# Optimization experiments

Measured on AMD Instinct MI355X. Metric: run time of the kernel, lower is better.

Reference implementation:

```python
import jax, jax.numpy as jnp
import numpy as np

B, T, D = 2, 2048, 1024
H, M = 8, 64
KD = D // H   # head_k_dim = head_v_dim = 128
EPS = 1e-5
GATE_NORM = 16.0


def setup_inputs() -> dict:
    key = jax.random.key(0)
    ks = jax.random.split(key, 7)
    sc = 0.02  # ~ xavier_uniform with gain 2**-2.5
    return {
        "hidden_states": jax.random.normal(ks[0], (B, T, D), jnp.float32),
        "Wq": jax.random.normal(ks[1], (D, D), jnp.float32) * sc,
        "Wk": jax.random.normal(ks[2], (D, D), jnp.float32) * sc,
        "Wv": jax.random.normal(ks[3], (D, D), jnp.float32) * sc,
        "Wf": jax.random.normal(ks[4], (H * M, D), jnp.float32) * sc,
        "Wo": jax.random.normal(ks[5], (D, D), jnp.float32) * sc,
        "g_weight": jnp.ones((D,), jnp.float32),
    }


def swish(x):
    return x * jax.nn.sigmoid(x)


def gated_abc_scan(q, k, v, s, g):
    """Gated ABC slot-memory recurrence.
    q,k: [B,H,T,K]; v: [B,H,T,V]; s,g: [B,H,T,M] (g is log forget gate).
    hk_t = hk_{t-1}*exp(g_t) + k_t (x) s_t            [B,H,K,M]
    p_t  = softmax(scale * q_t . hk_t, over slots M)
    hv_t = hv_{t-1}*exp(g_t) + s_t (x) v_t            [B,H,M,V]
    o_t  = p_t . hv_t
    """
    scale = q.shape[-1] ** -0.5
    qT = jnp.moveaxis(q, 2, 0) * scale  # [T,B,H,K]
    kT = jnp.moveaxis(k, 2, 0)
    vT = jnp.moveaxis(v, 2, 0)
    sT = jnp.moveaxis(s, 2, 0)
    gT = jnp.moveaxis(g, 2, 0)
    Bb, Hh, _, K = q.shape
    V, Mm = v.shape[-1], s.shape[-1]
    hk0 = jnp.zeros((Bb, Hh, K, Mm), q.dtype)
    hv0 = jnp.zeros((Bb, Hh, Mm, V), q.dtype)

    def step(carry, xs):
        hk, hv = carry
        qi, ki, vi, si, gi = xs
        ge = jnp.exp(gi)  # [B,H,M]
        hk = hk * ge[..., None, :] + ki[..., None] * si[..., None, :]
        p = jax.nn.softmax(jnp.einsum('bhk,bhkm->bhm', qi, hk), axis=-1)
        hv = hv * ge[..., None] + si[..., None] * vi[..., None, :]
        oi = jnp.einsum('bhm,bhmv->bhv', p, hv)
        return (hk, hv), oi

    _, oT = jax.lax.scan(step, (hk0, hv0), (qT, kT, vT, sT, gT))
    return jnp.moveaxis(oT, 0, 2)  # [B,H,T,V]


def reference(hidden_states, Wq, Wk, Wv, Wf, Wo, g_weight):
    x = hidden_states
    q = x @ Wq.T   # [B,T,D]
    k = x @ Wk.T
    v = x @ Wv.T
    f = x @ Wf.T   # [B,T,H*M]

    # b t (h d) -> b h t d
    q = jnp.moveaxis(q.reshape(B, T, H, KD), 2, 1)
    k = jnp.moveaxis(k.reshape(B, T, H, KD), 2, 1)
    v = jnp.moveaxis(v.reshape(B, T, H, KD), 2, 1)
    f = jnp.moveaxis(f.reshape(B, T, H, M), 2, 1)

    # feature map: swish on q, k, v
    q, k, v = swish(q), swish(k), swish(v)

    # log forget gate and input gate
    g = jax.nn.log_sigmoid(f) / GATE_NORM   # [B,H,T,M], <= 0
    s = 1.0 - jnp.exp(g)

    o = gated_abc_scan(q, k, v, s, g)       # [B,H,T,KD]
    o = jnp.moveaxis(o, 1, 2).reshape(B, T, D)  # b h t d -> b t (h d)

    # use_norm and not use_output_gate: swish -> RMSNorm(weight) -> o_proj
    o = swish(o)
    rms = o * jax.lax.rsqrt(jnp.mean(o * o, axis=-1, keepdims=True) + EPS)
    o = (rms * g_weight) @ Wo.T
    return o
```

## Files before the change

kernel.cpp:

```cpp
#include <hip/hip_runtime.h>
#include <cstddef>
#include <cstdint>

namespace {

constexpr int Bc = 2, Tc = 2048, Dc = 1024, Hc = 8, Mc = 64, KDc = 128;
constexpr int ROWS = Bc * Tc;
constexpr int CH = 64, NC = Tc / CH;
constexpr float SCALE = 0.08838834764831845f;
constexpr float GATE_NORM_INV = 1.0f / 16.0f;

typedef __attribute__((ext_vector_type(8))) short bf16x8;
typedef __attribute__((ext_vector_type(4))) float f32x4;

__device__ __forceinline__ float swishf(float x) {
  return x / (1.0f + __expf(-x));
}
__device__ __forceinline__ float logsig16f(float x) {
  return (fminf(x, 0.f) - __logf(1.f + __expf(-fabsf(x)))) * GATE_NORM_INV;
}
__device__ __forceinline__ unsigned short f2bf(float f) {
  union { float f; unsigned u; } v; v.f = f;
  unsigned r = v.u + 0x7FFF + ((v.u >> 16) & 1);
  return (unsigned short)(r >> 16);
}
__device__ __forceinline__ void fma4(float a, const float4& b, float4& acc) {
  acc.x = fmaf(a, b.x, acc.x); acc.y = fmaf(a, b.y, acc.y);
  acc.z = fmaf(a, b.z, acc.z); acc.w = fmaf(a, b.w, acc.w);
}
__device__ __forceinline__ float dot4acc(const float4& a, const float4& b, float c) {
  c = fmaf(a.x, b.x, c); c = fmaf(a.y, b.y, c);
  c = fmaf(a.z, b.z, c); c = fmaf(a.w, b.w, c);
  return c;
}

#define GLOAD_LDS16(g, l) __builtin_amdgcn_global_load_lds( \
    (const __attribute__((address_space(1))) unsigned int*)(g), \
    (__attribute__((address_space(3))) unsigned int*)(l), 16, 0, 0)

__global__ __launch_bounds__(256)
void cvt_bf16_all(const float* __restrict__ x, const float* __restrict__ wq,
                  const float* __restrict__ wk, const float* __restrict__ wv,
                  const float* __restrict__ wf, const float* __restrict__ wo,
                  unsigned short* __restrict__ xb, unsigned short* __restrict__ wqkvf,
                  unsigned short* __restrict__ wob)
{
  long e = ((long)blockIdx.x * 256 + threadIdx.x) * 8;
  const float* src; unsigned short* dst; long off;
  if (e < 4194304L)      { src = x;  dst = xb;              off = e; }
  else if (e < 5242880L) { src = wq; dst = wqkvf;           off = e - 4194304L; }
  else if (e < 6291456L) { src = wk; dst = wqkvf + 1048576; off = e - 5242880L; }
  else if (e < 7340032L) { src = wv; dst = wqkvf + 2097152; off = e - 6291456L; }
  else if (e < 7864320L) { src = wf; dst = wqkvf + 3145728; off = e - 7340032L; }
  else                   { src = wo; dst = wob;             off = e - 7864320L; }
  float4 a = *(const float4*)(src + off);
  float4 b = *(const float4*)(src + off + 4);
  ushort4 h0, h1;
  h0.x = f2bf(a.x); h0.y = f2bf(a.y); h0.z = f2bf(a.z); h0.w = f2bf(a.w);
  h1.x = f2bf(b.x); h1.y = f2bf(b.y); h1.z = f2bf(b.z); h1.w = f2bf(b.w);
  *(ushort4*)(dst + off) = h0;
  *(ushort4*)(dst + off + 4) = h1;
}

template<int EPI>
__global__ __launch_bounds__(256)
void gemm_bt(const unsigned short* __restrict__ A, const unsigned short* __restrict__ Bm,
             float* __restrict__ C0, float* __restrict__ C1,
             float* __restrict__ C2, float* __restrict__ C3)
{
  __shared__ __align__(16) unsigned short As[128 * 32];
  __shared__ __align__(16) unsigned short Bs[128 * 32];
  const int tid = threadIdx.x;
  const int lane = tid & 63, w = tid >> 6;
  const int bcol = (int)blockIdx.x, brow = (int)blockIdx.y;
  const int wr = w >> 1, wc = w & 1;
  const int lrow = lane & 15, lk8 = (lane >> 4) << 3;

  const int srow = w * 32 + (lane >> 2);
  const int scol = (lane & 3) << 3;
  const unsigned short* Ag0 = A + (size_t)(brow * 128 + srow) * 1024 + scol;
  const unsigned short* Ag1 = Ag0 + (size_t)16 * 1024;
  const unsigned short* Bg0 = Bm + (size_t)(bcol * 128 + srow) * 1024 + scol;
  const unsigned short* Bg1 = Bg0 + (size_t)16 * 1024;
  unsigned short* Al0 = As + w * 1024;
  unsigned short* Al1 = As + w * 1024 + 512;
  unsigned short* Bl0 = Bs + w * 1024;
  unsigned short* Bl1 = Bs + w * 1024 + 512;

  f32x4 acc[4][4];
#pragma unroll
  for (int i = 0; i < 4; ++i)
#pragma unroll
    for (int j = 0; j < 4; ++j)
#pragma unroll
      for (int r = 0; r < 4; ++r) acc[i][j][r] = 0.f;

  for (int k0 = 0; k0 < 1024; k0 += 32) {
    __syncthreads();
    GLOAD_LDS16(Ag0 + k0, Al0);
    GLOAD_LDS16(Ag1 + k0, Al1);
    GLOAD_LDS16(Bg0 + k0, Bl0);
    GLOAD_LDS16(Bg1 + k0, Bl1);
    __syncthreads();

    bf16x8 av[4], bv[4];
#pragma unroll
    for (int i = 0; i < 4; ++i)
      av[i] = *(const bf16x8*)&As[(wr * 64 + i * 16 + lrow) * 32 + lk8];
#pragma unroll
    for (int j = 0; j < 4; ++j)
      bv[j] = *(const bf16x8*)&Bs[(wc * 64 + j * 16 + lrow) * 32 + lk8];
#pragma unroll
    for (int i = 0; i < 4; ++i)
#pragma unroll
      for (int j = 0; j < 4; ++j)
        acc[i][j] = __builtin_amdgcn_mfma_f32_16x16x32_bf16(av[i], bv[j], acc[i][j], 0, 0, 0);
  }

#pragma unroll
  for (int i = 0; i < 4; ++i) {
#pragma unroll
    for (int j = 0; j < 4; ++j) {
#pragma unroll
      for (int r = 0; r < 4; ++r) {
        int row = brow * 128 + wr * 64 + i * 16 + ((lane >> 4) << 2) + r;
        int n   = bcol * 128 + wc * 64 + j * 16 + (lane & 15);
        float v = acc[i][j][r];
        if (EPI == 0) {
          C0[(size_t)row * 1024 + n] = v;
        } else {
          if (n < 1024)      C0[(size_t)row * 1024 + n]          = swishf(v);
          else if (n < 2048) C1[(size_t)row * 1024 + (n - 1024)] = swishf(v);
          else if (n < 3072) C2[(size_t)row * 1024 + (n - 2048)] = swishf(v);
          else               C3[(size_t)row * 512  + (n - 3072)] = logsig16f(v);
        }
      }
    }
  }
}

__global__ __launch_bounds__(256)
void scan_phase1(const float* __restrict__ K_, const float* __restrict__ V_,
                 const float* __restrict__ G_, float* __restrict__ St,
                 float* __restrict__ Gc)
{
  __shared__ __align__(16) float uls[CH][68];
  __shared__ __align__(16) float Bb[CH][132];
  __shared__ float egcs[CH];
  const int tid = threadIdx.x;
  const int c = (int)blockIdx.x, bh = (int)blockIdx.y;
  const int b = bh >> 3, h = bh & 7;
  const int t0 = c * CH;

  {
    const int gr = tid >> 2, gc0 = (tid & 3) << 4;
    const float* gsrc = G_ + (size_t)(b * Tc + t0 + gr) * (Hc * Mc) + h * Mc + gc0;
#pragma unroll
    for (int j = 0; j < 4; ++j)
      *(float4*)&uls[gr][gc0 + 4 * j] = *(const float4*)(gsrc + 4 * j);
  }
  {
    const float* ksrc = K_ + (size_t)(b * Tc + t0) * Dc + h * KDc;
#pragma unroll
    for (int j = 0; j < 8; ++j) {
      int fi = tid + j * 256;
      int r = fi >> 5, cc = (fi & 31) << 2;
      *(float4*)&Bb[r][cc] = *(const float4*)(ksrc + (size_t)r * Dc + cc);
    }
  }
  __syncthreads();
  if (tid < CH) {
    float run = 0.f;
    for (int t = 0; t < CH; ++t) {
      float gv = uls[t][tid];
      run += gv;
      uls[t][tid] = (1.0f - __expf(gv)) * __expf(-run);
    }
    float eg = __expf(run);
    egcs[tid] = eg;
    Gc[((size_t)bh * NC + c) * CH + tid] = eg;
  }
  __syncthreads();
  const size_t stbase = ((size_t)bh * NC + c) * 16384;
  {
    const int k0 = (tid >> 3) << 2, m0 = (tid & 7) << 3;
    float4 acc[4][2];
#pragma unroll
    for (int i = 0; i < 4; ++i) { acc[i][0] = make_float4(0,0,0,0); acc[i][1] = make_float4(0,0,0,0); }
    for (int tau = 0; tau < CH; ++tau) {
      float4 kv = *(const float4*)&Bb[tau][k0];
      float4 u0 = *(const float4*)&uls[tau][m0];
      float4 u1 = *(const float4*)&uls[tau][m0 + 4];
      fma4(kv.x, u0, acc[0][0]); fma4(kv.x, u1, acc[0][1]);
      fma4(kv.y, u0, acc[1][0]); fma4(kv.y, u1, acc[1][1]);
      fma4(kv.z, u0, acc[2][0]); fma4(kv.z, u1, acc[2][1]);
      fma4(kv.w, u0, acc[3][0]); fma4(kv.w, u1, acc[3][1]);
    }
    float4 e0 = *(const float4*)&egcs[m0];
    float4 e1 = *(const float4*)&egcs[m0 + 4];
#pragma unroll
    for (int i = 0; i < 4; ++i) {
      float4 o0, o1;
      o0.x = acc[i][0].x * e0.x; o0.y = acc[i][0].y * e0.y; o0.z = acc[i][0].z * e0.z; o0.w = acc[i][0].w * e0.w;
      o1.x = acc[i][1].x * e1.x; o1.y = acc[i][1].y * e1.y; o1.z = acc[i][1].z * e1.z; o1.w = acc[i][1].w * e1.w;
      float* dst = St + stbase + (size_t)(k0 + i) * 64 + m0;
      *(float4*)dst = o0; *(float4*)(dst + 4) = o1;
    }
  }
  __syncthreads();
  {
    const float* vsrc = V_ + (size_t)(b * Tc + t0) * Dc + h * KDc;
#pragma unroll
    for (int j = 0; j < 8; ++j) {
      int fi = tid + j * 256;
      int r = fi >> 5, cc = (fi & 31) << 2;
      *(float4*)&Bb[r][cc] = *(const float4*)(vsrc + (size_t)r * Dc + cc);
    }
  }
  __syncthreads();
  {
    const int m0 = (tid >> 4) << 2, v0 = (tid & 15) << 3;
    float4 acc[4][2];
#pragma unroll
    for (int i = 0; i < 4; ++i) { acc[i][0] = make_float4(0,0,0,0); acc[i][1] = make_float4(0,0,0,0); }
    for (int tau = 0; tau < CH; ++tau) {
      float4 u4 = *(const float4*)&uls[tau][m0];
      float4 va = *(const float4*)&Bb[tau][v0];
      float4 vb = *(const float4*)&Bb[tau][v0 + 4];
      fma4(u4.x, va, acc[0][0]); fma4(u4.x, vb, acc[0][1]);
      fma4(u4.y, va, acc[1][0]); fma4(u4.y, vb, acc[1][1]);
      fma4(u4.z, va, acc[2][0]); fma4(u4.z, vb, acc[2][1]);
      fma4(u4.w, va, acc[3][0]); fma4(u4.w, vb, acc[3][1]);
    }
#pragma unroll
    for (int i = 0; i < 4; ++i) {
      float eg = egcs[m0 + i];
      float4 o0 = acc[i][0], o1 = acc[i][1];
      o0.x *= eg; o0.y *= eg; o0.z *= eg; o0.w *= eg;
      o1.x *= eg; o1.y *= eg; o1.z *= eg; o1.w *= eg;
      float* dst = St + stbase + 8192 + (size_t)(m0 + i) * 128 + v0;
      *(float4*)dst = o0; *(float4*)(dst + 4) = o1;
    }
  }
}

__global__ __launch_bounds__(256)
void scan_phase2(float* St, const float* __restrict__ Gc)
{
  const int tid = threadIdx.x;
  const int bh = (int)blockIdx.x, slice = (int)blockIdx.y;
  const int e0 = slice * 1024 + tid * 4;
  const bool isHk = e0 < 8192;
  float* base = St + (size_t)bh * NC * 16384 + e0;
  const float* gcp = Gc + (size_t)bh * NC * CH;
  float4 run = make_float4(0, 0, 0, 0);
  float4 d = *(float4*)base;
  for (int c = 0; c < NC; ++c) {
    float4 dn = make_float4(0, 0, 0, 0);
    if (c + 1 < NC) dn = *(float4*)(base + (size_t)(c + 1) * 16384);
    float4 ge;
    if (isHk) {
      ge = *(const float4*)(gcp + c * CH + (e0 & 63));
    } else {
      float g1 = gcp[c * CH + ((e0 - 8192) >> 7)];
      ge = make_float4(g1, g1, g1, g1);
    }
    *(float4*)(base + (size_t)c * 16384) = run;
    run.x = fmaf(run.x, ge.x, d.x);
    run.y = fmaf(run.y, ge.y, d.y);
    run.z = fmaf(run.z, ge.z, d.z);
    run.w = fmaf(run.w, ge.w, d.w);
    d = dn;
  }
}

__global__ __launch_bounds__(256)
void scan_phase3(const float* __restrict__ Q_, const float* __restrict__ K_,
                 const float* __restrict__ V_, const float* __restrict__ G_,
                 const float* __restrict__ St, float* __restrict__ O_)
{
  __shared__ __align__(16) float Qs[CH][132];
  __shared__ __align__(16) float Bf[8704];
  __shared__ __align__(16) float us[CH][68];
  __shared__ __align__(16) float es[CH][68];
  __shared__ __align__(16) float Ss[CH][68];
  __shared__ __align__(16) float Ps[CH][68];

  const int tid = threadIdx.x;
  const int c = (int)blockIdx.x, bh = (int)blockIdx.y;
  const int b = bh >> 3, h = bh & 7;
  const int t0 = c * CH;
  const size_t stbase = ((size_t)bh * NC + c) * 16384;

  {
    const int gr = tid >> 2, gc0 = (tid & 3) << 4;
    const float* gsrc = G_ + (size_t)(b * Tc + t0 + gr) * (Hc * Mc) + h * Mc + gc0;
#pragma unroll
    for (int j = 0; j < 4; ++j)
      *(float4*)&es[gr][gc0 + 4 * j] = *(const float4*)(gsrc + 4 * j);
    const float* qsrc = Q_ + (size_t)(b * Tc + t0) * Dc + h * KDc;
    const float* ksrc = K_ + (size_t)(b * Tc + t0) * Dc + h * KDc;
#pragma unroll
    for (int j = 0; j < 8; ++j) {
      int fi = tid + j * 256;
      int r = fi >> 5, cc4 = (fi & 31) << 2;
      *(float4*)&Qs[r][cc4] = *(const float4*)(qsrc + (size_t)r * Dc + cc4);
      *(float4*)&Bf[r * 132 + cc4] = *(const float4*)(ksrc + (size_t)r * Dc + cc4);
    }
  }
  __syncthreads();
  if (tid < CH) {
    float run = 0.f;
    for (int t = 0; t < CH; ++t) {
      float gv = es[t][tid];
      run += gv;
      us[t][tid] = (1.0f - __expf(gv)) * __expf(-run);
      es[t][tid] = __expf(run);
    }
  }
  const int tt = tid >> 4, ccg = tid & 15;
  {
    const int tr = tt << 2, tc = ccg << 2;
    float4 acc[4];
#pragma unroll
    for (int i = 0; i < 4; ++i) acc[i] = make_float4(0, 0, 0, 0);
    for (int k = 0; k < KDc; k += 4) {
      float4 kr0 = *(const float4*)&Bf[(tc + 0) * 132 + k];
      float4 kr1 = *(const float4*)&Bf[(tc + 1) * 132 + k];
      float4 kr2 = *(const float4*)&Bf[(tc + 2) * 132 + k];
      float4 kr3 = *(const float4*)&Bf[(tc + 3) * 132 + k];
#pragma unroll
      for (int i = 0; i < 4; ++i) {
        float4 qi = *(const float4*)&Qs[tr + i][k];
        acc[i].x = dot4acc(qi, kr0, acc[i].x);
        acc[i].y = dot4acc(qi, kr1, acc[i].y);
        acc[i].z = dot4acc(qi, kr2, acc[i].z);
        acc[i].w = dot4acc(qi, kr3, acc[i].w);
      }
    }
#pragma unroll
    for (int i = 0; i < 4; ++i) {
      float4 w;
      w.x = (tc + 0 <= tr + i) ? acc[i].x : 0.f;
      w.y = (tc + 1 <= tr + i) ? acc[i].y : 0.f;
      w.z = (tc + 2 <= tr + i) ? acc[i].z : 0.f;
      w.w = (tc + 3 <= tr + i) ? acc[i].w : 0.f;
      *(float4*)&Ss[tr + i][tc] = w;
    }
  }
  __syncthreads();
  {
#pragma unroll
    for (int j = 0; j < 8; ++j) {
      int fi = tid + j * 256;
      int k = fi >> 4, m4 = (fi & 15) << 2;
      *(float4*)&Bf[k * 68 + m4] = *(const float4*)(St + stbase + (size_t)k * 64 + m4);
    }
  }
  __syncthreads();
  {
    const int tr = tt << 2, m0 = ccg << 2;
    float4 acc[4];
#pragma unroll
    for (int i = 0; i < 4; ++i) acc[i] = make_float4(0, 0, 0, 0);
    for (int tau = 0; tau < CH; tau += 4) {
      float4 u0 = *(const float4*)&us[tau + 0][m0];
      float4 u1 = *(const float4*)&us[tau + 1][m0];
      float4 u2 = *(const float4*)&us[tau + 2][m0];
      float4 u3 = *(const float4*)&us[tau + 3][m0];
#pragma unroll
      for (int i = 0; i < 4; ++i) {
        float4 s4 = *(const float4*)&Ss[tr + i][tau];
        fma4(s4.x, u0, acc[i]); fma4(s4.y, u1, acc[i]);
        fma4(s4.z, u2, acc[i]); fma4(s4.w, u3, acc[i]);
      }
    }
    for (int k = 0; k < KDc; k += 4) {
      float4 h0 = *(const float4*)&Bf[(k + 0) * 68 + m0];
      float4 h1 = *(const float4*)&Bf[(k + 1) * 68 + m0];
      float4 h2 = *(const float4*)&Bf[(k + 2) * 68 + m0];
      float4 h3 = *(const float4*)&Bf[(k + 3) * 68 + m0];
#pragma unroll
      for (int i = 0; i < 4; ++i) {
        float4 q4 = *(const float4*)&Qs[tr + i][k];
        fma4(q4.x, h0, acc[i]); fma4(q4.y, h1, acc[i]);
        fma4(q4.z, h2, acc[i]); fma4(q4.w, h3, acc[i]);
      }
    }
#pragma unroll
    for (int i = 0; i < 4; ++i) {
      float4 ev = *(const float4*)&es[tr + i][m0];
      float4 ov;
      ov.x = SCALE * ev.x * acc[i].x;
      ov.y = SCALE * ev.y * acc[i].y;
      ov.z = SCALE * ev.z * acc[i].z;
      ov.w = SCALE * ev.w * acc[i].w;
      *(float4*)&Ps[tr + i][m0] = ov;
    }
  }
  __syncthreads();
  {
    const int row = tid >> 2, m0 = (tid & 3) << 4;
    float4 a0 = *(const float4*)&Ps[row][m0];
    float4 a1 = *(const float4*)&Ps[row][m0 + 4];
    float4 a2 = *(const float4*)&Ps[row][m0 + 8];
    float4 a3 = *(const float4*)&Ps[row][m0 + 12];
    float mx = fmaxf(fmaxf(fmaxf(a0.x, a0.y), fmaxf(a0.z, a0.w)),
                     fmaxf(fmaxf(a1.x, a1.y), fmaxf(a1.z, a1.w)));
    mx = fmaxf(mx, fmaxf(fmaxf(fmaxf(a2.x, a2.y), fmaxf(a2.z, a2.w)),
                         fmaxf(fmaxf(a3.x, a3.y), fmaxf(a3.z, a3.w))));
    mx = fmaxf(mx, __shfl_xor(mx, 1, 64));
    mx = fmaxf(mx, __shfl_xor(mx, 2, 64));
    a0.x = __expf(a0.x - mx); a0.y = __expf(a0.y - mx); a0.z = __expf(a0.z - mx); a0.w = __expf(a0.w - mx);
    a1.x = __expf(a1.x - mx); a1.y = __expf(a1.y - mx); a1.z = __expf(a1.z - mx); a1.w = __expf(a1.w - mx);
    a2.x = __expf(a2.x - mx); a2.y = __expf(a2.y - mx); a2.z = __expf(a2.z - mx); a2.w = __expf(a2.w - mx);
    a3.x = __expf(a3.x - mx); a3.y = __expf(a3.y - mx); a3.z = __expf(a3.z - mx); a3.w = __expf(a3.w - mx);
    float sm = a0.x + a0.y + a0.z + a0.w + a1.x + a1.y + a1.z + a1.w
             + a2.x + a2.y + a2.z + a2.w + a3.x + a3.y + a3.z + a3.w;
    sm += __shfl_xor(sm, 1, 64);
    sm += __shfl_xor(sm, 2, 64);
    float inv = 1.0f / sm;
    float4 e0 = *(const float4*)&es[row][m0];
    float4 e1 = *(const float4*)&es[row][m0 + 4];
    float4 e2 = *(const float4*)&es[row][m0 + 8];
    float4 e3 = *(const float4*)&es[row][m0 + 12];
    a0.x *= inv * e0.x; a0.y *= inv * e0.y; a0.z *= inv * e0.z; a0.w *= inv * e0.w;
    a1.x *= inv * e1.x; a1.y *= inv * e1.y; a1.z *= inv * e1.z; a1.w *= inv * e1.w;
    a2.x *= inv * e2.x; a2.y *= inv * e2.y; a2.z *= inv * e2.z; a2.w *= inv * e2.w;
    a3.x *= inv * e3.x; a3.y *= inv * e3.y; a3.z *= inv * e3.z; a3.w *= inv * e3.w;
    *(float4*)&Ss[row][m0] = a0;
    *(float4*)&Ss[row][m0 + 4] = a1;
    *(float4*)&Ss[row][m0 + 8] = a2;
    *(float4*)&Ss[row][m0 + 12] = a3;
  }
  {
    const float* vsrc = V_ + (size_t)(b * Tc + t0) * Dc + h * KDc;
#pragma unroll
    for (int j = 0; j < 8; ++j) {
      int fi = tid + j * 256;
      int r = fi >> 5, cc4 = (fi & 31) << 2;
      *(float4*)&Bf[r * 132 + cc4] = *(const float4*)(vsrc + (size_t)r * Dc + cc4);
    }
  }
  __syncthreads();
  {
    const int tr = tt << 2, tc = ccg << 2;
    float4 acc[4];
#pragma unroll
    for (int i = 0; i < 4; ++i) acc[i] = make_float4(0, 0, 0, 0);
    for (int m = 0; m < CH; m += 4) {
      float4 u0 = *(const float4*)&us[tc + 0][m];
      float4 u1 = *(const float4*)&us[tc + 1][m];
      float4 u2 = *(const float4*)&us[tc + 2][m];
      float4 u3 = *(const float4*)&us[tc + 3][m];
#pragma unroll
      for (int i = 0; i < 4; ++i) {
        float4 w4 = *(const float4*)&Ss[tr + i][m];
        acc[i].x = dot4acc(w4, u0, acc[i].x);
        acc[i].y = dot4acc(w4, u1, acc[i].y);
        acc[i].z = dot4acc(w4, u2, acc[i].z);
        acc[i].w = dot4acc(w4, u3, acc[i].w);
      }
    }
#pragma unroll
    for (int i = 0; i < 4; ++i) {
      float4 w;
      w.x = (tc + 0 <= tr + i) ? acc[i].x : 0.f;
      w.y = (tc + 1 <= tr + i) ? acc[i].y : 0.f;
      w.z = (tc + 2 <= tr + i) ? acc[i].z : 0.f;
      w.w = (tc + 3 <= tr + i) ? acc[i].w : 0.f;
      *(float4*)&Ps[tr + i][tc] = w;
    }
  }
  __syncthreads();
  const int tr = tt << 2, v0 = ccg << 3;
  float4 accO[4][2];
#pragma unroll
  for (int i = 0; i < 4; ++i) { accO[i][0] = make_float4(0,0,0,0); accO[i][1] = make_float4(0,0,0,0); }
  for (int tau = 0; tau < CH; tau += 4) {
    float4 pr[4];
#pragma unroll
    for (int i = 0; i < 4; ++i) pr[i] = *(const float4*)&Ps[tr + i][tau];
#pragma unroll
    for (int d = 0; d < 4; ++d) {
      float4 va = *(const float4*)&Bf[(tau + d) * 132 + v0];
      float4 vb = *(const float4*)&Bf[(tau + d) * 132 + v0 + 4];
#pragma unroll
      for (int i = 0; i < 4; ++i) {
        float p = (d == 0) ? pr[i].x : (d == 1) ? pr[i].y : (d == 2) ? pr[i].z : pr[i].w;
        fma4(p, va, accO[i][0]); fma4(p, vb, accO[i][1]);
      }
    }
  }
  __syncthreads();
  {
#pragma unroll
    for (int j = 0; j < 8; ++j) {
      int fi = tid + j * 256;
      int m = fi >> 5, c4 = (fi & 31) << 2;
      *(float4*)&Bf[m * 132 + c4] = *(const float4*)(St + stbase + 8192 + (size_t)m * 128 + c4);
    }
  }
  __syncthreads();
  for (int m = 0; m < CH; m += 4) {
    float4 wr[4];
#pragma unroll
    for (int i = 0; i < 4; ++i) wr[i] = *(const float4*)&Ss[tr + i][m];
#pragma unroll
    for (int d = 0; d < 4; ++d) {
      float4 ha = *(const float4*)&Bf[(m + d) * 132 + v0];
      float4 hb = *(const float4*)&Bf[(m + d) * 132 + v0 + 4];
#pragma unroll
      for (int i = 0; i < 4; ++i) {
        float w = (d == 0) ? wr[i].x : (d == 1) ? wr[i].y : (d == 2) ? wr[i].z : wr[i].w;
        fma4(w, ha, accO[i][0]); fma4(w, hb, accO[i][1]);
      }
    }
  }
#pragma unroll
  for (int i = 0; i < 4; ++i) {
    float* dst = O_ + (size_t)(b * Tc + t0 + tr + i) * Dc + h * KDc + v0;
    *(float4*)dst = accO[i][0];
    *(float4*)(dst + 4) = accO[i][1];
  }
}

__global__ __launch_bounds__(256)
void post_rms(const float* __restrict__ Oin, const float* __restrict__ gw,
              unsigned short* __restrict__ Nout)
{
  __shared__ float red[4];
  const int row = (int)blockIdx.x, tid = threadIdx.x;
  const float4 o4 = *(const float4*)(Oin + (size_t)row * Dc + tid * 4);
  float4 s4;
  s4.x = swishf(o4.x); s4.y = swishf(o4.y); s4.z = swishf(o4.z); s4.w = swishf(o4.w);
  float ss = s4.x * s4.x + s4.y * s4.y + s4.z * s4.z + s4.w * s4.w;
#pragma unroll
  for (int off = 32; off > 0; off >>= 1) ss += __shfl_xor(ss, off, 64);
  if ((tid & 63) == 0) red[tid >> 6] = ss;
  __syncthreads();
  float total = red[0] + red[1] + red[2] + red[3];
  float rms = rsqrtf(total * (1.0f / Dc) + 1e-5f);
  const float4 g4 = *(const float4*)(gw + tid * 4);
  ushort4 h;
  h.x = f2bf(s4.x * rms * g4.x);
  h.y = f2bf(s4.y * rms * g4.y);
  h.z = f2bf(s4.z * rms * g4.z);
  h.w = f2bf(s4.w * rms * g4.w);
  *(ushort4*)(Nout + (size_t)row * Dc + tid * 4) = h;
}

}

extern "C" void kernel_launch(void* const* d_in, const int* in_sizes, int n_in,
                              void* d_out, int out_size, void* d_ws, size_t ws_size,
                              hipStream_t stream)
{
  const float* x  = (const float*)d_in[0];
  const float* Wq = (const float*)d_in[1];
  const float* Wk = (const float*)d_in[2];
  const float* Wv = (const float*)d_in[3];
  const float* Wf = (const float*)d_in[4];
  const float* Wo = (const float*)d_in[5];
  const float* gw = (const float*)d_in[6];
  float* out = (float*)d_out;

  char* ws = (char*)d_ws;
  const size_t MB = 1ull << 20;
  float* qb  = (float*)(ws);
  float* kb  = (float*)(ws + 16 * MB);
  float* vb  = (float*)(ws + 32 * MB);
  float* gb  = (float*)(ws + 48 * MB);
  float* st  = (float*)(ws + 56 * MB);
  float* gcb = (float*)(ws + 88 * MB);
  float* ob  = (float*)(ws + 89 * MB);
  unsigned short* xb    = (unsigned short*)(ws + 56 * MB);
  unsigned short* wqkvf = (unsigned short*)(ws + 64 * MB);
  unsigned short* wob   = (unsigned short*)(ws + 105 * MB);
  unsigned short* nbb   = (unsigned short*)(ws);

  dim3 blk(256);
  cvt_bf16_all<<<dim3(4352), blk, 0, stream>>>(x, Wq, Wk, Wv, Wf, Wo, xb, wqkvf, wob);
  gemm_bt<1><<<dim3(28, 32), blk, 0, stream>>>(xb, wqkvf, qb, kb, vb, gb);
  scan_phase1<<<dim3(NC, 16), blk, 0, stream>>>(kb, vb, gb, st, gcb);
  scan_phase2<<<dim3(16, 16), blk, 0, stream>>>(st, gcb);
  scan_phase3<<<dim3(NC, 16), blk, 0, stream>>>(qb, kb, vb, gb, st, ob);
  post_rms<<<dim3(ROWS), blk, 0, stream>>>(ob, gw, nbb);
  gemm_bt<0><<<dim3(8, 32), blk, 0, stream>>>(nbb, wob, out, nullptr, nullptr, nullptr);
}
```

Baseline: 318.2 us.

## Move chunked scan intra-chunk matmuls to bf16 MFMA with transposed state layout

Rewrites scan_phase3 so its intra-chunk products (QK^T, S·u, Q·hk, W·u, P·V, W·hv) run as bf16 16x16x32 MFMA ops instead of scalar fp32 FMA loops. Inputs and chunk states are converted to bf16 in LDS. To give MFMA operands a contiguous K dimension, phase1 now stores chunk states transposed (hk as [M][K], hv as [V][M]), and phase2's gate indexing is changed to match. The goal is to cut the cost of the FP32 ALU work in the per-chunk kernel. In exchange it loses precision from bf16 rounding of activations, states and probabilities, and adds conversion overhead and scattered scalar output stores.

New measurement: 266.9 us. 1.19x faster.

```diff
diff --git a/kernel.cpp b/kernel.cpp
--- a/kernel.cpp
+++ b/kernel.cpp
@@ -28,10 +28,8 @@
   acc.x = fmaf(a, b.x, acc.x); acc.y = fmaf(a, b.y, acc.y);
   acc.z = fmaf(a, b.z, acc.z); acc.w = fmaf(a, b.w, acc.w);
 }
-__device__ __forceinline__ float dot4acc(const float4& a, const float4& b, float c) {
-  c = fmaf(a.x, b.x, c); c = fmaf(a.y, b.y, c);
-  c = fmaf(a.z, b.z, c); c = fmaf(a.w, b.w, c);
-  return c;
+__device__ __forceinline__ float getc(const float4& v, int c) {
+  return (c == 0) ? v.x : (c == 1) ? v.y : (c == 2) ? v.z : v.w;
 }
 
 #define GLOAD_LDS16(g, l) __builtin_amdgcn_global_load_lds( \
@@ -196,15 +194,16 @@
       fma4(kv.z, u0, acc[2][0]); fma4(kv.z, u1, acc[2][1]);
       fma4(kv.w, u0, acc[3][0]); fma4(kv.w, u1, acc[3][1]);
     }
-    float4 e0 = *(const float4*)&egcs[m0];
-    float4 e1 = *(const float4*)&egcs[m0 + 4];
-#pragma unroll
-    for (int i = 0; i < 4; ++i) {
-      float4 o0, o1;
-      o0.x = acc[i][0].x * e0.x; o0.y = acc[i][0].y * e0.y; o0.z = acc[i][0].z * e0.z; o0.w = acc[i][0].w * e0.w;
-      o1.x = acc[i][1].x * e1.x; o1.y = acc[i][1].y * e1.y; o1.z = acc[i][1].z * e1.z; o1.w = acc[i][1].w * e1.w;
-      float* dst = St + stbase + (size_t)(k0 + i) * 64 + m0;
-      *(float4*)dst = o0; *(float4*)(dst + 4) = o1;
+#pragma unroll
+    for (int jm = 0; jm < 8; ++jm) {
+      int m = m0 + jm, hh = jm >> 2, cc = jm & 3;
+      float eg = egcs[m];
+      float4 o;
+      o.x = getc(acc[0][hh], cc) * eg;
+      o.y = getc(acc[1][hh], cc) * eg;
+      o.z = getc(acc[2][hh], cc) * eg;
+      o.w = getc(acc[3][hh], cc) * eg;
+      *(float4*)(St + stbase + (size_t)m * 128 + k0) = o;
     }
   }
   __syncthreads();
@@ -232,14 +231,16 @@
       fma4(u4.z, va, acc[2][0]); fma4(u4.z, vb, acc[2][1]);
       fma4(u4.w, va, acc[3][0]); fma4(u4.w, vb, acc[3][1]);
     }
-#pragma unroll
-    for (int i = 0; i < 4; ++i) {
-      float eg = egcs[m0 + i];
-      float4 o0 = acc[i][0], o1 = acc[i][1];
-      o0.x *= eg; o0.y *= eg; o0.z *= eg; o0.w *= eg;
-      o1.x *= eg; o1.y *= eg; o1.z *= eg; o1.w *= eg;
-      float* dst = St + stbase + 8192 + (size_t)(m0 + i) * 128 + v0;
-      *(float4*)dst = o0; *(float4*)(dst + 4) = o1;
+    float4 e4 = *(const float4*)&egcs[m0];
+#pragma unroll
+    for (int jv = 0; jv < 8; ++jv) {
+      int v = v0 + jv, hh = jv >> 2, cc = jv & 3;
+      float4 o;
+      o.x = getc(acc[0][hh], cc) * e4.x;
+      o.y = getc(acc[1][hh], cc) * e4.y;
+      o.z = getc(acc[2][hh], cc) * e4.z;
+      o.w = getc(acc[3][hh], cc) * e4.w;
+      *(float4*)(St + stbase + 8192 + (size_t)v * 64 + m0) = o;
     }
   }
 }
@@ -260,10 +261,10 @@
     if (c + 1 < NC) dn = *(float4*)(base + (size_t)(c + 1) * 16384);
     float4 ge;
     if (isHk) {
-      ge = *(const float4*)(gcp + c * CH + (e0 & 63));
+      float g1 = gcp[c * CH + (e0 >> 7)];
+      ge = make_float4(g1, g1, g1, g1);
     } else {
-      float g1 = gcp[c * CH + ((e0 - 8192) >> 7)];
-      ge = make_float4(g1, g1, g1, g1);
+      ge = *(const float4*)(gcp + c * CH + ((e0 - 8192) & 63));
     }
     *(float4*)(base + (size_t)c * 16384) = run;
     run.x = fmaf(run.x, ge.x, d.x);
@@ -279,250 +280,228 @@
                  const float* __restrict__ V_, const float* __restrict__ G_,
                  const float* __restrict__ St, float* __restrict__ O_)
 {
-  __shared__ __align__(16) float Qs[CH][132];
-  __shared__ __align__(16) float Bf[8704];
-  __shared__ __align__(16) float us[CH][68];
-  __shared__ __align__(16) float es[CH][68];
-  __shared__ __align__(16) float Ss[CH][68];
-  __shared__ __align__(16) float Ps[CH][68];
-
-  const int tid = threadIdx.x;
+  __shared__ __align__(16) unsigned short Qb[64 * 136];
+  __shared__ __align__(16) unsigned short buf2[128 * 72];
+  __shared__ __align__(16) unsigned short Sb[64 * 72];
+  __shared__ __align__(16) unsigned short Wb[64 * 72];
+  __shared__ __align__(16) unsigned short P2b[64 * 72];
+  __shared__ __align__(16) unsigned short ub[64 * 72];
+  __shared__ __align__(16) unsigned short ubt[64 * 72];
+  __shared__ __align__(16) float es[64 * 68];
+
+  const int tid = threadIdx.x, lane = tid & 63, w = tid >> 6;
   const int c = (int)blockIdx.x, bh = (int)blockIdx.y;
   const int b = bh >> 3, h = bh & 7;
   const int t0 = c * CH;
   const size_t stbase = ((size_t)bh * NC + c) * 16384;
-
-  {
-    const int gr = tid >> 2, gc0 = (tid & 3) << 4;
-    const float* gsrc = G_ + (size_t)(b * Tc + t0 + gr) * (Hc * Mc) + h * Mc + gc0;
-#pragma unroll
-    for (int j = 0; j < 4; ++j)
-      *(float4*)&es[gr][gc0 + 4 * j] = *(const float4*)(gsrc + 4 * j);
-    const float* qsrc = Q_ + (size_t)(b * Tc + t0) * Dc + h * KDc;
-    const float* ksrc = K_ + (size_t)(b * Tc + t0) * Dc + h * KDc;
+  const int col = lane & 15, rb = (lane >> 4) << 2;
+  const int arow = lane & 15, ak = (lane >> 4) << 3;
+
+  {
+    const int r = tid >> 2, cs = (tid & 3) << 5;
+    const float* qs = Q_ + (size_t)(b * Tc + t0 + r) * Dc + h * KDc + cs;
+    const float* ks = K_ + (size_t)(b * Tc + t0 + r) * Dc + h * KDc + cs;
+#pragma unroll
+    for (int q = 0; q < 8; ++q) {
+      float4 a = *(const float4*)(qs + q * 4);
+      ushort4 ha; ha.x = f2bf(a.x); ha.y = f2bf(a.y); ha.z = f2bf(a.z); ha.w = f2bf(a.w);
+      *(ushort4*)&Qb[r * 136 + cs + q * 4] = ha;
+      float4 bq = *(const float4*)(ks + q * 4);
+      ushort4 hb; hb.x = f2bf(bq.x); hb.y = f2bf(bq.y); hb.z = f2bf(bq.z); hb.w = f2bf(bq.w);
+      *(ushort4*)&buf2[r * 136 + cs + q * 4] = hb;
+    }
+    const int gcs = (tid & 3) << 4;
+    const float* gs = G_ + (size_t)(b * Tc + t0 + r) * (Hc * Mc) + h * Mc + gcs;
+#pragma unroll
+    for (int q = 0; q < 4; ++q)
+      *(float4*)&es[r * 68 + gcs + q * 4] = *(const float4*)(gs + q * 4);
+  }
+  __syncthreads();
+  if (tid < 64) {
+    float run = 0.f;
+    ushort4 pk;
+    for (int t = 0; t < 64; ++t) {
+      float gv = es[t * 68 + tid];
+      run += gv;
+      float uu = (1.0f - __expf(gv)) * __expf(-run);
+      es[t * 68 + tid] = __expf(run);
+      unsigned short ubf = f2bf(uu);
+      ub[t * 72 + tid] = ubf;
+      ((unsigned short*)&pk)[t & 3] = ubf;
+      if ((t & 3) == 3) *(ushort4*)&ubt[tid * 72 + (t - 3)] = pk;
+    }
+  }
+  __syncthreads();
+  {
+    f32x4 s[4];
+#pragma unroll
+    for (int j = 0; j < 4; ++j)
+#pragma unroll
+      for (int r = 0; r < 4; ++r) s[j][r] = 0.f;
+#pragma unroll
+    for (int k0 = 0; k0 < 128; k0 += 32) {
+      bf16x8 aq = *(const bf16x8*)&Qb[(w * 16 + arow) * 136 + k0 + ak];
+#pragma unroll
+      for (int j = 0; j < 4; ++j) {
+        bf16x8 bk = *(const bf16x8*)&buf2[(j * 16 + arow) * 136 + k0 + ak];
+        s[j] = __builtin_amdgcn_mfma_f32_16x16x32_bf16(aq, bk, s[j], 0, 0, 0);
+      }
+    }
+#pragma unroll
+    for (int j = 0; j < 4; ++j)
+#pragma unroll
+      for (int r = 0; r < 4; ++r) {
+        int t = w * 16 + rb + r, tau = j * 16 + col;
+        Sb[t * 72 + tau] = f2bf((tau <= t) ? s[j][r] : 0.f);
+      }
+  }
+  __syncthreads();
+  {
+    const int r = tid >> 2, cs = (tid & 3) << 5;
+    const float* hs = St + stbase + (size_t)r * 128 + cs;
+#pragma unroll
+    for (int q = 0; q < 8; ++q) {
+      float4 a = *(const float4*)(hs + q * 4);
+      ushort4 ha; ha.x = f2bf(a.x); ha.y = f2bf(a.y); ha.z = f2bf(a.z); ha.w = f2bf(a.w);
+      *(ushort4*)&buf2[r * 136 + cs + q * 4] = ha;
+    }
+  }
+  __syncthreads();
+  {
+    f32x4 a4[4];
+#pragma unroll
+    for (int j = 0; j < 4; ++j)
+#pragma unroll
+      for (int r = 0; r < 4; ++r) a4[j][r] = 0.f;
+#pragma unroll
+    for (int k0 = 0; k0 < 64; k0 += 32) {
+      bf16x8 as_ = *(const bf16x8*)&Sb[(w * 16 + arow) * 72 + k0 + ak];
+#pragma unroll
+      for (int j = 0; j < 4; ++j) {
+        bf16x8 bu = *(const bf16x8*)&ubt[(j * 16 + arow) * 72 + k0 + ak];
+        a4[j] = __builtin_amdgcn_mfma_f32_16x16x32_bf16(as_, bu, a4[j], 0, 0, 0);
+      }
+    }
+#pragma unroll
+    for (int k0 = 0; k0 < 128; k0 += 32) {
+      bf16x8 aq = *(const bf16x8*)&Qb[(w * 16 + arow) * 136 + k0 + ak];
+#pragma unroll
+      for (int j = 0; j < 4; ++j) {
+        bf16x8 bh_ = *(const bf16x8*)&buf2[(j * 16 + arow) * 136 + k0 + ak];
+        a4[j] = __builtin_amdgcn_mfma_f32_16x16x32_bf16(aq, bh_, a4[j], 0, 0, 0);
+      }
+    }
+    float er[4][4], lg[4][4];
+#pragma unroll
+    for (int j = 0; j < 4; ++j)
+#pragma unroll
+      for (int r = 0; r < 4; ++r) {
+        er[j][r] = es[(w * 16 + rb + r) * 68 + j * 16 + col];
+        lg[j][r] = SCALE * er[j][r] * a4[j][r];
+      }
+    float mx[4] = {-1e30f, -1e30f, -1e30f, -1e30f};
+#pragma unroll
+    for (int j = 0; j < 4; ++j)
+#pragma unroll
+      for (int r = 0; r < 4; ++r) mx[r] = fmaxf(mx[r], lg[j][r]);
+#pragma unroll
+    for (int bx = 1; bx < 16; bx <<= 1)
+#pragma unroll
+      for (int r = 0; r < 4; ++r) mx[r] = fmaxf(mx[r], __shfl_xor(mx[r], bx, 64));
+    float se[4] = {0.f, 0.f, 0.f, 0.f}, p[4][4];
+#pragma unroll
+    for (int j = 0; j < 4; ++j)
+#pragma unroll
+      for (int r = 0; r < 4; ++r) { p[j][r] = __expf(lg[j][r] - mx[r]); se[r] += p[j][r]; }
+#pragma unroll
+    for (int bx = 1; bx < 16; bx <<= 1)
+#pragma unroll
+      for (int r = 0; r < 4; ++r) se[r] += __shfl_xor(se[r], bx, 64);
+#pragma unroll
+    for (int j = 0; j < 4; ++j)
+#pragma unroll
+      for (int r = 0; r < 4; ++r) {
+        float wv = p[j][r] / se[r] * er[j][r];
+        Wb[(w * 16 + rb + r) * 72 + j * 16 + col] = f2bf(wv);
+      }
+  }
+  __syncthreads();
+  {
+#pragma unroll
+    for (int q = 0; q < 8; ++q) {
+      int fi = tid + q * 256;
+      int tau = fi & 63, v0 = (fi >> 6) << 2;
+      float4 a = *(const float4*)(V_ + (size_t)(b * Tc + t0 + tau) * Dc + h * KDc + v0);
+      buf2[(v0 + 0) * 72 + tau] = f2bf(a.x);
+      buf2[(v0 + 1) * 72 + tau] = f2bf(a.y);
+      buf2[(v0 + 2) * 72 + tau] = f2bf(a.z);
+      buf2[(v0 + 3) * 72 + tau] = f2bf(a.w);
+    }
+  }
+  {
+    f32x4 p2[4];
+#pragma unroll
+    for (int j = 0; j < 4; ++j)
+#pragma unroll
+      for (int r = 0; r < 4; ++r) p2[j][r] = 0.f;
+#pragma unroll
+    for (int k0 = 0; k0 < 64; k0 += 32) {
+      bf16x8 aw = *(const bf16x8*)&Wb[(w * 16 + arow) * 72 + k0 + ak];
+#pragma unroll
+      for (int j = 0; j < 4; ++j) {
+        bf16x8 bu = *(const bf16x8*)&ub[(j * 16 + arow) * 72 + k0 + ak];
+        p2[j] = __builtin_amdgcn_mfma_f32_16x16x32_bf16(aw, bu, p2[j], 0, 0, 0);
+      }
+    }
+#pragma unroll
+    for (int j = 0; j < 4; ++j)
+#pragma unroll
+      for (int r = 0; r < 4; ++r) {
+        int t = w * 16 + rb + r, tau = j * 16 + col;
+        P2b[t * 72 + tau] = f2bf((tau <= t) ? p2[j][r] : 0.f);
+      }
+  }
+  __syncthreads();
+  f32x4 o8[8];
+#pragma unroll
+  for (int j = 0; j < 8; ++j)
+#pragma unroll
+    for (int r = 0; r < 4; ++r) o8[j][r] = 0.f;
+#pragma unroll
+  for (int k0 = 0; k0 < 64; k0 += 32) {
+    bf16x8 ap = *(const bf16x8*)&P2b[(w * 16 + arow) * 72 + k0 + ak];
 #pragma unroll
     for (int j = 0; j < 8; ++j) {
-      int fi = tid + j * 256;
-      int r = fi >> 5, cc4 = (fi & 31) << 2;
-      *(float4*)&Qs[r][cc4] = *(const float4*)(qsrc + (size_t)r * Dc + cc4);
-      *(float4*)&Bf[r * 132 + cc4] = *(const float4*)(ksrc + (size_t)r * Dc + cc4);
-    }
-  }
-  __syncthreads();
-  if (tid < CH) {
-    float run = 0.f;
-    for (int t = 0; t < CH; ++t) {
-      float gv = es[t][tid];
-      run += gv;
-      us[t][tid] = (1.0f - __expf(gv)) * __expf(-run);
-      es[t][tid] = __expf(run);
-    }
-  }
-  const int tt = tid >> 4, ccg = tid & 15;
-  {
-    const int tr = tt << 2, tc = ccg << 2;
-    float4 acc[4];
-#pragma unroll
-    for (int i = 0; i < 4; ++i) acc[i] = make_float4(0, 0, 0, 0);
-    for (int k = 0; k < KDc; k += 4) {
-      float4 kr0 = *(const float4*)&Bf[(tc + 0) * 132 + k];
-      float4 kr1 = *(const float4*)&Bf[(tc + 1) * 132 + k];
-      float4 kr2 = *(const float4*)&Bf[(tc + 2) * 132 + k];
-      float4 kr3 = *(const float4*)&Bf[(tc + 3) * 132 + k];
-#pragma unroll
-      for (int i = 0; i < 4; ++i) {
-        float4 qi = *(const float4*)&Qs[tr + i][k];
-        acc[i].x = dot4acc(qi, kr0, acc[i].x);
-        acc[i].y = dot4acc(qi, kr1, acc[i].y);
-        acc[i].z = dot4acc(qi, kr2, acc[i].z);
-        acc[i].w = dot4acc(qi, kr3, acc[i].w);
-      }
-    }
-#pragma unroll
-    for (int i = 0; i < 4; ++i) {
-      float4 w;
-      w.x = (tc + 0 <= tr + i) ? acc[i].x : 0.f;
-      w.y = (tc + 1 <= tr + i) ? acc[i].y : 0.f;
-      w.z = (tc + 2 <= tr + i) ? acc[i].z : 0.f;
-      w.w = (tc + 3 <= tr + i) ? acc[i].w : 0.f;
-      *(float4*)&Ss[tr + i][tc] = w;
-    }
-  }
-  __syncthreads();
-  {
+      bf16x8 bv = *(const bf16x8*)&buf2[(j * 16 + arow) * 72 + k0 + ak];
+      o8[j] = __builtin_amdgcn_mfma_f32_16x16x32_bf16(ap, bv, o8[j], 0, 0, 0);
+    }
+  }
+  __syncthreads();
+  {
+    const int r = tid >> 1, cs = (tid & 1) << 5;
+    const float* hs = St + stbase + 8192 + (size_t)r * 64 + cs;
+#pragma unroll
+    for (int q = 0; q < 8; ++q) {
+      float4 a = *(const float4*)(hs + q * 4);
+      ushort4 ha; ha.x = f2bf(a.x); ha.y = f2bf(a.y); ha.z = f2bf(a.z); ha.w = f2bf(a.w);
+      *(ushort4*)&buf2[r * 72 + cs + q * 4] = ha;
+    }
+  }
+  __syncthreads();
+#pragma unroll
+  for (int k0 = 0; k0 < 64; k0 += 32) {
+    bf16x8 aw = *(const bf16x8*)&Wb[(w * 16 + arow) * 72 + k0 + ak];
 #pragma unroll
     for (int j = 0; j < 8; ++j) {
-      int fi = tid + j * 256;
-      int k = fi >> 4, m4 = (fi & 15) << 2;
-      *(float4*)&Bf[k * 68 + m4] = *(const float4*)(St + stbase + (size_t)k * 64 + m4);
-    }
-  }
-  __syncthreads();
-  {
-    const int tr = tt << 2, m0 = ccg << 2;
-    float4 acc[4];
-#pragma unroll
-    for (int i = 0; i < 4; ++i) acc[i] = make_float4(0, 0, 0, 0);
-    for (int tau = 0; tau < CH; tau += 4) {
-      float4 u0 = *(const float4*)&us[tau + 0][m0];
-      float4 u1 = *(const float4*)&us[tau + 1][m0];
-      float4 u2 = *(const float4*)&us[tau + 2][m0];
-      float4 u3 = *(const float4*)&us[tau + 3][m0];
-#pragma unroll
-      for (int i = 0; i < 4; ++i) {
-        float4 s4 = *(const float4*)&Ss[tr + i][tau];
-        fma4(s4.x, u0, acc[i]); fma4(s4.y, u1, acc[i]);
-        fma4(s4.z, u2, acc[i]); fma4(s4.w, u3, acc[i]);
-      }
-    }
-    for (int k = 0; k < KDc; k += 4) {
-      float4 h0 = *(const float4*)&Bf[(k + 0) * 68 + m0];
-      float4 h1 = *(const float4*)&Bf[(k + 1) * 68 + m0];
-      float4 h2 = *(const float4*)&Bf[(k + 2) * 68 + m0];
-      float4 h3 = *(const float4*)&Bf[(k + 3) * 68 + m0];
-#pragma unroll
-      for (int i = 0; i < 4; ++i) {
-        float4 q4 = *(const float4*)&Qs[tr + i][k];
-        fma4(q4.x, h0, acc[i]); fma4(q4.y, h1, acc[i]);
-        fma4(q4.z, h2, acc[i]); fma4(q4.w, h3, acc[i]);
-      }
-    }
-#pragma unroll
-    for (int i = 0; i < 4; ++i) {
-      float4 ev = *(const float4*)&es[tr + i][m0];
-      float4 ov;
-      ov.x = SCALE * ev.x * acc[i].x;
-      ov.y = SCALE * ev.y * acc[i].y;
-      ov.z = SCALE * ev.z * acc[i].z;
-      ov.w = SCALE * ev.w * acc[i].w;
-      *(float4*)&Ps[tr + i][m0] = ov;
-    }
-  }
-  __syncthreads();
-  {
-    const int row = tid >> 2, m0 = (tid & 3) << 4;
-    float4 a0 = *(const float4*)&Ps[row][m0];
-    float4 a1 = *(const float4*)&Ps[row][m0 + 4];
-    float4 a2 = *(const float4*)&Ps[row][m0 + 8];
-    float4 a3 = *(const float4*)&Ps[row][m0 + 12];
-    float mx = fmaxf(fmaxf(fmaxf(a0.x, a0.y), fmaxf(a0.z, a0.w)),
-                     fmaxf(fmaxf(a1.x, a1.y), fmaxf(a1.z, a1.w)));
-    mx = fmaxf(mx, fmaxf(fmaxf(fmaxf(a2.x, a2.y), fmaxf(a2.z, a2.w)),
-                         fmaxf(fmaxf(a3.x, a3.y), fmaxf(a3.z, a3.w))));
-    mx = fmaxf(mx, __shfl_xor(mx, 1, 64));
-    mx = fmaxf(mx, __shfl_xor(mx, 2, 64));
-    a0.x = __expf(a0.x - mx); a0.y = __expf(a0.y - mx); a0.z = __expf(a0.z - mx); a0.w = __expf(a0.w - mx);
-    a1.x = __expf(a1.x - mx); a1.y = __expf(a1.y - mx); a1.z = __expf(a1.z - mx); a1.w = __expf(a1.w - mx);
-    a2.x = __expf(a2.x - mx); a2.y = __expf(a2.y - mx); a2.z = __expf(a2.z - mx); a2.w = __expf(a2.w - mx);
-    a3.x = __expf(a3.x - mx); a3.y = __expf(a3.y - mx); a3.z = __expf(a3.z - mx); a3.w = __expf(a3.w - mx);
-    float sm = a0.x + a0.y + a0.z + a0.w + a1.x + a1.y + a1.z + a1.w
-             + a2.x + a2.y + a2.z + a2.w + a3.x + a3.y + a3.z + a3.w;
-    sm += __shfl_xor(sm, 1, 64);
-    sm += __shfl_xor(sm, 2, 64);
-    float inv = 1.0f / sm;
-    float4 e0 = *(const float4*)&es[row][m0];
-    float4 e1 = *(const float4*)&es[row][m0 + 4];
-    float4 e2 = *(const float4*)&es[row][m0 + 8];
-    float4 e3 = *(const float4*)&es[row][m0 + 12];
-    a0.x *= inv * e0.x; a0.y *= inv * e0.y; a0.z *= inv * e0.z; a0.w *= inv * e0.w;
-    a1.x *= inv * e1.x; a1.y *= inv * e1.y; a1.z *= inv * e1.z; a1.w *= inv * e1.w;
-    a2.x *= inv * e2.x; a2.y *= inv * e2.y; a2.z *= inv * e2.z; a2.w *= inv * e2.w;
-    a3.x *= inv * e3.x; a3.y *= inv * e3.y; a3.z *= inv * e3.z; a3.w *= inv * e3.w;
-    *(float4*)&Ss[row][m0] = a0;
-    *(float4*)&Ss[row][m0 + 4] = a1;
-    *(float4*)&Ss[row][m0 + 8] = a2;
-    *(float4*)&Ss[row][m0 + 12] = a3;
-  }
-  {
-    const float* vsrc = V_ + (size_t)(b * Tc + t0) * Dc + h * KDc;
-#pragma unroll
-    for (int j = 0; j < 8; ++j) {
-      int fi = tid + j * 256;
-      int r = fi >> 5, cc4 = (fi & 31) << 2;
-      *(float4*)&Bf[r * 132 + cc4] = *(const float4*)(vsrc + (size_t)r * Dc + cc4);
-    }
-  }
-  __syncthreads();
-  {
-    const int tr = tt << 2, tc = ccg << 2;
-    float4 acc[4];
-#pragma unroll
-    for (int i = 0; i < 4; ++i) acc[i] = make_float4(0, 0, 0, 0);
-    for (int m = 0; m < CH; m += 4) {
-      float4 u0 = *(const float4*)&us[tc + 0][m];
-      float4 u1 = *(const float4*)&us[tc + 1][m];
-      float4 u2 = *(const float4*)&us[tc + 2][m];
-      float4 u3 = *(const float4*)&us[tc + 3][m];
-#pragma unroll
-      for (int i = 0; i < 4; ++i) {
-        float4 w4 = *(const float4*)&Ss[tr + i][m];
-        acc[i].x = dot4acc(w4, u0, acc[i].x);
-        acc[i].y = dot4acc(w4, u1, acc[i].y);
-        acc[i].z = dot4acc(w4, u2, acc[i].z);
-        acc[i].w = dot4acc(w4, u3, acc[i].w);
-      }
-    }
-#pragma unroll
-    for (int i = 0; i < 4; ++i) {
-      float4 w;
-      w.x = (tc + 0 <= tr + i) ? acc[i].x : 0.f;
-      w.y = (tc + 1 <= tr + i) ? acc[i].y : 0.f;
-      w.z = (tc + 2 <= tr + i) ? acc[i].z : 0.f;
-      w.w = (tc + 3 <= tr + i) ? acc[i].w : 0.f;
-      *(float4*)&Ps[tr + i][tc] = w;
-    }
-  }
-  __syncthreads();
-  const int tr = tt << 2, v0 = ccg << 3;
-  float4 accO[4][2];
-#pragma unroll
-  for (int i = 0; i < 4; ++i) { accO[i][0] = make_float4(0,0,0,0); accO[i][1] = make_float4(0,0,0,0); }
-  for (int tau = 0; tau < CH; tau += 4) {
-    float4 pr[4];
-#pragma unroll
-    for (int i = 0; i < 4; ++i) pr[i] = *(const float4*)&Ps[tr + i][tau];
-#pragma unroll
-    for (int d = 0; d < 4; ++d) {
-      float4 va = *(const float4*)&Bf[(tau + d) * 132 + v0];
-      float4 vb = *(const float4*)&Bf[(tau + d) * 132 + v0 + 4];
-#pragma unroll
-      for (int i = 0; i < 4; ++i) {
-        float p = (d == 0) ? pr[i].x : (d == 1) ? pr[i].y : (d == 2) ? pr[i].z : pr[i].w;
-        fma4(p, va, accO[i][0]); fma4(p, vb, accO[i][1]);
-      }
-    }
-  }
-  __syncthreads();
-  {
-#pragma unroll
-    for (int j = 0; j < 8; ++j) {
-      int fi = tid + j * 256;
-      int m = fi >> 5, c4 = (fi & 31) << 2;
-      *(float4*)&Bf[m * 132 + c4] = *(const float4*)(St + stbase + 8192 + (size_t)m * 128 + c4);
-    }
-  }
-  __syncthreads();
-  for (int m = 0; m < CH; m += 4) {
-    float4 wr[4];
-#pragma unroll
-    for (int i = 0; i < 4; ++i) wr[i] = *(const float4*)&Ss[tr + i][m];
-#pragma unroll
-    for (int d = 0; d < 4; ++d) {
-      float4 ha = *(const float4*)&Bf[(m + d) * 132 + v0];
-      float4 hb = *(const float4*)&Bf[(m + d) * 132 + v0 + 4];
-#pragma unroll
-      for (int i = 0; i < 4; ++i) {
-        float w = (d == 0) ? wr[i].x : (d == 1) ? wr[i].y : (d == 2) ? wr[i].z : wr[i].w;
-        fma4(w, ha, accO[i][0]); fma4(w, hb, accO[i][1]);
-      }
-    }
-  }
-#pragma unroll
-  for (int i = 0; i < 4; ++i) {
-    float* dst = O_ + (size_t)(b * Tc + t0 + tr + i) * Dc + h * KDc + v0;
-    *(float4*)dst = accO[i][0];
-    *(float4*)(dst + 4) = accO[i][1];
-  }
+      bf16x8 bhv = *(const bf16x8*)&buf2[(j * 16 + arow) * 72 + k0 + ak];
+      o8[j] = __builtin_amdgcn_mfma_f32_16x16x32_bf16(aw, bhv, o8[j], 0, 0, 0);
+    }
+  }
+#pragma unroll
+  for (int j = 0; j < 8; ++j)
+#pragma unroll
+    for (int r = 0; r < 4; ++r)
+      O_[(size_t)(b * Tc + t0 + w * 16 + rb + r) * Dc + h * KDc + j * 16 + col] = o8[j][r];
 }
 
 __global__ __launch_bounds__(256)
```
